# Performance work log

Measured on AMD Instinct MI355X. Metric: run time of the kernel, lower is better.

## Reference

```python
import jax, jax.numpy as jnp
import numpy as np

N_NODES = 100000
N_EDGES = 1200000
D = 64
N_REL = 50


def setup_inputs() -> dict:
    key = jax.random.key(0)
    ks = jax.random.split(key, 7)
    x = jax.random.normal(ks[0], (N_NODES, D), dtype=jnp.float32)
    rel_weight = jax.random.normal(ks[1], (N_REL, D), dtype=jnp.float32)
    loop_w1 = jax.random.normal(ks[2], (D, D), dtype=jnp.float32) * (1.0 / np.sqrt(D))
    loop_w2 = jax.random.normal(ks[3], (D, D), dtype=jnp.float32) * (1.0 / np.sqrt(D))
    src = jax.random.randint(ks[4], (N_EDGES,), 0, N_NODES, dtype=jnp.int32)
    dst = jax.random.randint(ks[5], (N_EDGES,), 0, N_NODES, dtype=jnp.int32)
    etype = jax.random.randint(ks[6], (N_EDGES,), 0, N_REL, dtype=jnp.int32)
    return {"x": x, "rel_weight": rel_weight, "loop_w1": loop_w1,
            "loop_w2": loop_w2, "src": src, "dst": dst, "etype": etype}


def _rgcn_layer(x, loop_w, rel_weight, src, dst, etype, n_nodes):
    # norm='both': pre-scale source feats by out_degree^-0.5
    ones_e = jnp.ones(src.shape[0], dtype=x.dtype)
    out_deg = jax.ops.segment_sum(ones_e, src, num_segments=n_nodes)
    in_deg = jax.ops.segment_sum(ones_e, dst, num_segments=n_nodes)
    norm_out = jnp.maximum(out_deg, 1.0) ** -0.5          # [N]
    h_src = x * norm_out[:, None]                          # [N, D]
    # per-edge: gather src feats + relation weights, elementwise multiply
    m = h_src[src] * rel_weight[etype]                     # [E, D]
    # scatter-mean over destination nodes
    msum = jax.ops.segment_sum(m, dst, num_segments=n_nodes)  # [N, D]
    mix = msum / jnp.maximum(in_deg, 1.0)[:, None]
    # self-loop dense matmul on dst feats (= original x)
    rst = x @ loop_w + mix
    # post-scale by in_degree^-0.5
    rst = rst * (jnp.maximum(in_deg, 1.0) ** -0.5)[:, None]
    return jax.nn.relu(rst)


def reference(x, rel_weight, loop_w1, loop_w2, src, dst, etype):
    n = x.shape[0]
    h = _rgcn_layer(x, loop_w1, rel_weight, src, dst, etype, n)
    h = _rgcn_layer(h, loop_w2, rel_weight, src, dst, etype, n)
    return h
```

## Files before the change

### kernel.cpp

```cpp
#include <hip/hip_runtime.h>


#define SCAN_BLK 1024

__global__ void deg_kernel(const int* __restrict__ src, const int* __restrict__ dst,
                           int* __restrict__ out_cnt, int* __restrict__ in_cnt, int E) {
  int i = blockIdx.x * blockDim.x + threadIdx.x;
  int stride = gridDim.x * blockDim.x;
  for (int e = i; e < E; e += stride) {
    atomicAdd(&out_cnt[src[e]], 1);
    atomicAdd(&in_cnt[dst[e]], 1);
  }
}

__global__ void scan_a(const int* __restrict__ in, int* __restrict__ out1,
                       int* __restrict__ bsums, int n) {
  __shared__ int tmp[SCAN_BLK];
  int i = blockIdx.x * SCAN_BLK + threadIdx.x;
  tmp[threadIdx.x] = (i < n) ? in[i] : 0;
  __syncthreads();
  for (int off = 1; off < SCAN_BLK; off <<= 1) {
    int t = (threadIdx.x >= off) ? tmp[threadIdx.x - off] : 0;
    __syncthreads();
    tmp[threadIdx.x] += t;
    __syncthreads();
  }
  if (i < n) out1[i] = tmp[threadIdx.x];
  if (threadIdx.x == SCAN_BLK - 1) bsums[blockIdx.x] = tmp[SCAN_BLK - 1];
}

__global__ void scan_b(const int* __restrict__ bsums, int* __restrict__ boff, int nb) {
  __shared__ int t[256];
  int v = (threadIdx.x < nb) ? bsums[threadIdx.x] : 0;
  t[threadIdx.x] = v;
  __syncthreads();
  for (int off = 1; off < 256; off <<= 1) {
    int u = (threadIdx.x >= off) ? t[threadIdx.x - off] : 0;
    __syncthreads();
    t[threadIdx.x] += u;
    __syncthreads();
  }
  if (threadIdx.x < nb) boff[threadIdx.x] = t[threadIdx.x] - v;
}

__global__ void scan_c(int* __restrict__ rowptr, const int* __restrict__ boff, int n) {
  int i = blockIdx.x * blockDim.x + threadIdx.x;
  if (i < n) rowptr[i + 1] += boff[i >> 10];
  if (i == 0) rowptr[0] = 0;
}

__global__ void norms_kernel(const int* __restrict__ out_cnt, const int* __restrict__ in_cnt,
                             const int* __restrict__ rowptr,
                             float4* __restrict__ nrm4, int* __restrict__ cursor, int n) {
  int i = blockIdx.x * blockDim.x + threadIdx.x;
  if (i < n) {
    float od = (float)max(out_cnt[i], 1);
    float id = (float)max(in_cnt[i], 1);
    float4 v;
    v.x = 1.0f / id;
    v.y = sqrtf(od);
    v.z = rsqrtf(id);
    v.w = rsqrtf(od);
    nrm4[i] = v;
    cursor[i] = rowptr[i];
  }
}

__global__ void prescale_kernel(const float4* __restrict__ x4, const float4* __restrict__ nrm4,
                                float4* __restrict__ xs4, int n16) {
  int i = blockIdx.x * blockDim.x + threadIdx.x;
  if (i < n16) {
    float no = nrm4[i >> 4].w;
    float4 v = x4[i];
    v.x *= no; v.y *= no; v.z *= no; v.w *= no;
    xs4[i] = v;
  }
}

__global__ void fill_csr(const int* __restrict__ src, const int* __restrict__ dst,
                         const int* __restrict__ et, int* __restrict__ cursor,
                         int* __restrict__ ce, int E) {
  int i = blockIdx.x * blockDim.x + threadIdx.x;
  int stride = gridDim.x * blockDim.x;
  for (int e = i; e < E; e += stride) {
    int d = dst[e];
    int pos = atomicAdd(&cursor[d], 1);
    ce[pos] = src[e] | (et[e] << 20);
  }
}

template <bool FINAL>
__launch_bounds__(256, 8)
__global__ void layer_kernel(const float* __restrict__ xs, const float* __restrict__ W,
                             const float* __restrict__ relw,
                             const int* __restrict__ rowptr, const int* __restrict__ ce,
                             const float4* __restrict__ nrm4,
                             float* __restrict__ xout, int n) {
  __shared__ float Wl[4096];
  {
    const float4* __restrict__ Wg = (const float4*)W;
    float4* Wl4 = (float4*)Wl;
    for (int i = threadIdx.x; i < 1024; i += 256) Wl4[i] = Wg[i];
  }
  __syncthreads();

  const int node = blockIdx.x * 4 + (threadIdx.x >> 6);
  if (node >= n) return;
  const int lane = threadIdx.x & 63;
  const int g = lane >> 4;
  const int l = lane & 15;

  const int rb = rowptr[node];
  const int re = rowptr[node + 1];
  const float4 nr = nrm4[node];

  const float4* __restrict__ xs4 = (const float4*)xs;
  const float4* __restrict__ rw4 = (const float4*)relw;

  float4 acc0 = {0.f, 0.f, 0.f, 0.f};
  float4 acc1 = {0.f, 0.f, 0.f, 0.f};
  int e = rb + g;
  for (; e + 4 < re; e += 8) {
    const int p0 = ce[e];
    const int p1 = ce[e + 4];
    const int s0 = p0 & 0xFFFFF, t0 = p0 >> 20;
    const int s1 = p1 & 0xFFFFF, t1 = p1 >> 20;
    const float4 xv0 = xs4[(size_t)s0 * 16 + l];
    const float4 xv1 = xs4[(size_t)s1 * 16 + l];
    const float4 rv0 = rw4[t0 * 16 + l];
    const float4 rv1 = rw4[t1 * 16 + l];
    acc0.x = fmaf(xv0.x, rv0.x, acc0.x);
    acc0.y = fmaf(xv0.y, rv0.y, acc0.y);
    acc0.z = fmaf(xv0.z, rv0.z, acc0.z);
    acc0.w = fmaf(xv0.w, rv0.w, acc0.w);
    acc1.x = fmaf(xv1.x, rv1.x, acc1.x);
    acc1.y = fmaf(xv1.y, rv1.y, acc1.y);
    acc1.z = fmaf(xv1.z, rv1.z, acc1.z);
    acc1.w = fmaf(xv1.w, rv1.w, acc1.w);
  }
  if (e < re) {
    const int p = ce[e];
    const int s = p & 0xFFFFF, t = p >> 20;
    const float4 xv = xs4[(size_t)s * 16 + l];
    const float4 rv = rw4[t * 16 + l];
    acc0.x = fmaf(xv.x, rv.x, acc0.x);
    acc0.y = fmaf(xv.y, rv.y, acc0.y);
    acc0.z = fmaf(xv.z, rv.z, acc0.z);
    acc0.w = fmaf(xv.w, rv.w, acc0.w);
  }
  float4 pre;
  pre.x = acc0.x + acc1.x;
  pre.y = acc0.y + acc1.y;
  pre.z = acc0.z + acc1.z;
  pre.w = acc0.w + acc1.w;

  pre.x += __shfl_xor(pre.x, 16); pre.x += __shfl_xor(pre.x, 32);
  pre.y += __shfl_xor(pre.y, 16); pre.y += __shfl_xor(pre.y, 32);
  pre.z += __shfl_xor(pre.z, 16); pre.z += __shfl_xor(pre.z, 32);
  pre.w += __shfl_xor(pre.w, 16); pre.w += __shfl_xor(pre.w, 32);

  const int srcl = lane >> 2;
  const float t0 = __shfl(pre.x, srcl);
  const float t1 = __shfl(pre.y, srcl);
  const float t2 = __shfl(pre.z, srcl);
  const float t3 = __shfl(pre.w, srcl);
  const float ea = (lane & 2) ? ((lane & 1) ? t3 : t2)
                              : ((lane & 1) ? t1 : t0);

  float d0 = 0.f, d1 = 0.f, d2 = 0.f, d3 = 0.f;
  const float* __restrict__ xrow = xs + (size_t)node * 64;
#pragma unroll
  for (int k = 0; k < 64; k += 4) {
    d0 = fmaf(xrow[k],     Wl[(k)     * 64 + lane], d0);
    d1 = fmaf(xrow[k + 1], Wl[(k + 1) * 64 + lane], d1);
    d2 = fmaf(xrow[k + 2], Wl[(k + 2) * 64 + lane], d2);
    d3 = fmaf(xrow[k + 3], Wl[(k + 3) * 64 + lane], d3);
  }
  const float dense = (d0 + d1) + (d2 + d3);

  const float scale = FINAL ? nr.z : nr.z * nr.w;
  const float r = fmaf(ea, nr.x, dense * nr.y) * scale;
  xout[(size_t)node * 64 + lane] = fmaxf(r, 0.f);
}

extern "C" void kernel_launch(void* const* d_in, const int* in_sizes, int n_in,
                              void* d_out, int out_size, void* d_ws, size_t ws_size,
                              hipStream_t stream) {
  const float* x     = (const float*)d_in[0];
  const float* relw  = (const float*)d_in[1];
  const float* w1    = (const float*)d_in[2];
  const float* w2    = (const float*)d_in[3];
  const int*   src   = (const int*)d_in[4];
  const int*   dst   = (const int*)d_in[5];
  const int*   etype = (const int*)d_in[6];

  const int N = in_sizes[0] / 64;
  const int E = in_sizes[4];

  char* w = (char*)d_ws;
  size_t off = 0;
  auto alloc = [&](size_t bytes) -> void* {
    void* p = w + off;
    off = (off + bytes + 255) & ~(size_t)255;
    return p;
  };
  int*    out_cnt = (int*)alloc((size_t)N * 4);
  int*    in_cnt  = (int*)alloc((size_t)N * 4);
  int*    rowptr  = (int*)alloc((size_t)(N + 1) * 4);
  int*    cursor  = (int*)alloc((size_t)N * 4);
  float4* nrm4    = (float4*)alloc((size_t)N * 16);
  int*    bsums   = (int*)alloc(256 * 4);
  int*    boff    = (int*)alloc(256 * 4);
  int*    ce      = (int*)alloc((size_t)E * 4);
  float*  xs      = (float*)alloc((size_t)N * 64 * 4);
  float*  h1s     = (float*)alloc((size_t)N * 64 * 4);

  hipMemsetAsync(out_cnt, 0, ((char*)rowptr - (char*)out_cnt), stream);

  const int nb = (N + SCAN_BLK - 1) / SCAN_BLK;

  deg_kernel<<<4096, 256, 0, stream>>>(src, dst, out_cnt, in_cnt, E);
  scan_a<<<nb, SCAN_BLK, 0, stream>>>(in_cnt, rowptr + 1, bsums, N);
  scan_b<<<1, 256, 0, stream>>>(bsums, boff, nb);
  scan_c<<<(N + 255) / 256, 256, 0, stream>>>(rowptr, boff, N);
  norms_kernel<<<(N + 255) / 256, 256, 0, stream>>>(out_cnt, in_cnt, rowptr, nrm4, cursor, N);
  prescale_kernel<<<(N * 16 + 255) / 256, 256, 0, stream>>>((const float4*)x, nrm4,
                                                            (float4*)xs, N * 16);
  fill_csr<<<4096, 256, 0, stream>>>(src, dst, etype, cursor, ce, E);

  const int lblocks = (N + 3) / 4;
  layer_kernel<false><<<lblocks, 256, 0, stream>>>(xs, w1, relw, rowptr, ce, nrm4, h1s, N);
  layer_kernel<true><<<lblocks, 256, 0, stream>>>(h1s, w2, relw, rowptr, ce, nrm4,
                                                  (float*)d_out, N);
}
```

Before: 465.4 us.

## Split self-loop matmul into separate register-resident kernel; merge scan fixup with norms

Moves the dense self-loop x@W product out of the gather layer kernel into a persistent kernel that holds one column of W in registers per lane and writes a pre-scaled intermediate y. The layer kernel then reads y instead of loading W into 16KB of shared memory per block, which removes the shared-memory staging and barrier and should allow higher occupancy for the latency-bound gather. It also fuses the scan fixup with the norms/cursor kernel by writing a separate rowfin array. The cost is two extra kernel launches and an extra N×64 float write and read per layer.

```diff
diff --git a/kernel.cpp b/kernel.cpp
--- a/kernel.cpp
+++ b/kernel.cpp
@@ -43,17 +43,16 @@
   if (threadIdx.x < nb) boff[threadIdx.x] = t[threadIdx.x] - v;
 }
 
-__global__ void scan_c(int* __restrict__ rowptr, const int* __restrict__ boff, int n) {
-  int i = blockIdx.x * blockDim.x + threadIdx.x;
-  if (i < n) rowptr[i + 1] += boff[i >> 10];
-  if (i == 0) rowptr[0] = 0;
-}
-
-__global__ void norms_kernel(const int* __restrict__ out_cnt, const int* __restrict__ in_cnt,
-                             const int* __restrict__ rowptr,
-                             float4* __restrict__ nrm4, int* __restrict__ cursor, int n) {
+__global__ void scan_c2(const int* __restrict__ rowptr, const int* __restrict__ boff,
+                        const int* __restrict__ out_cnt, const int* __restrict__ in_cnt,
+                        int* __restrict__ rowfin, int* __restrict__ cursor,
+                        float4* __restrict__ nrm4, int n) {
   int i = blockIdx.x * blockDim.x + threadIdx.x;
   if (i < n) {
+    rowfin[i + 1] = rowptr[i + 1] + boff[i >> 10];
+    int rp0 = (i == 0) ? 0 : rowptr[i] + boff[(i - 1) >> 10];
+    if (i == 0) rowfin[0] = 0;
+    cursor[i] = rp0;
     float od = (float)max(out_cnt[i], 1);
     float id = (float)max(in_cnt[i], 1);
     float4 v;
@@ -62,7 +61,6 @@
     v.z = rsqrtf(id);
     v.w = rsqrtf(od);
     nrm4[i] = v;
-    cursor[i] = rowptr[i];
   }
 }
 
@@ -89,21 +87,38 @@
   }
 }
 
+__launch_bounds__(256, 4)
+__global__ void selfloop_kernel(const float* __restrict__ xs, const float* __restrict__ W,
+                                const float4* __restrict__ nrm4,
+                                float* __restrict__ y, int n) {
+  const int lane = threadIdx.x & 63;
+  float wc[64];
+#pragma unroll
+  for (int k = 0; k < 64; ++k) wc[k] = W[k * 64 + lane];
+  const int wid = (blockIdx.x * blockDim.x + threadIdx.x) >> 6;
+  const int nw = (gridDim.x * blockDim.x) >> 6;
+  for (int node0 = wid; node0 < n; node0 += nw) {
+    const int node = __builtin_amdgcn_readfirstlane(node0);
+    const float* __restrict__ xrow = xs + (size_t)node * 64;
+    float d0 = 0.f, d1 = 0.f, d2 = 0.f, d3 = 0.f;
+#pragma unroll
+    for (int k = 0; k < 64; k += 4) {
+      d0 = fmaf(xrow[k],     wc[k],     d0);
+      d1 = fmaf(xrow[k + 1], wc[k + 1], d1);
+      d2 = fmaf(xrow[k + 2], wc[k + 2], d2);
+      d3 = fmaf(xrow[k + 3], wc[k + 3], d3);
+    }
+    y[(size_t)node * 64 + lane] = ((d0 + d1) + (d2 + d3)) * nrm4[node].y;
+  }
+}
+
 template <bool FINAL>
 __launch_bounds__(256, 8)
-__global__ void layer_kernel(const float* __restrict__ xs, const float* __restrict__ W,
+__global__ void layer_kernel(const float* __restrict__ xs, const float* __restrict__ y,
                              const float* __restrict__ relw,
                              const int* __restrict__ rowptr, const int* __restrict__ ce,
                              const float4* __restrict__ nrm4,
                              float* __restrict__ xout, int n) {
-  __shared__ float Wl[4096];
-  {
-    const float4* __restrict__ Wg = (const float4*)W;
-    float4* Wl4 = (float4*)Wl;
-    for (int i = threadIdx.x; i < 1024; i += 256) Wl4[i] = Wg[i];
-  }
-  __syncthreads();
-
   const int node = blockIdx.x * 4 + (threadIdx.x >> 6);
   if (node >= n) return;
   const int lane = threadIdx.x & 63;
@@ -167,19 +182,10 @@
   const float ea = (lane & 2) ? ((lane & 1) ? t3 : t2)
                               : ((lane & 1) ? t1 : t0);
 
-  float d0 = 0.f, d1 = 0.f, d2 = 0.f, d3 = 0.f;
-  const float* __restrict__ xrow = xs + (size_t)node * 64;
-#pragma unroll
-  for (int k = 0; k < 64; k += 4) {
-    d0 = fmaf(xrow[k],     Wl[(k)     * 64 + lane], d0);
-    d1 = fmaf(xrow[k + 1], Wl[(k + 1) * 64 + lane], d1);
-    d2 = fmaf(xrow[k + 2], Wl[(k + 2) * 64 + lane], d2);
-    d3 = fmaf(xrow[k + 3], Wl[(k + 3) * 64 + lane], d3);
-  }
-  const float dense = (d0 + d1) + (d2 + d3);
+  const float yv = y[(size_t)node * 64 + lane];
 
   const float scale = FINAL ? nr.z : nr.z * nr.w;
-  const float r = fmaf(ea, nr.x, dense * nr.y) * scale;
+  const float r = fmaf(ea, nr.x, yv) * scale;
   xout[(size_t)node * 64 + lane] = fmaxf(r, 0.f);
 }
 
@@ -207,6 +213,7 @@
   int*    out_cnt = (int*)alloc((size_t)N * 4);
   int*    in_cnt  = (int*)alloc((size_t)N * 4);
   int*    rowptr  = (int*)alloc((size_t)(N + 1) * 4);
+  int*    rowfin  = (int*)alloc((size_t)(N + 1) * 4);
   int*    cursor  = (int*)alloc((size_t)N * 4);
   float4* nrm4    = (float4*)alloc((size_t)N * 16);
   int*    bsums   = (int*)alloc(256 * 4);
@@ -214,6 +221,7 @@
   int*    ce      = (int*)alloc((size_t)E * 4);
   float*  xs      = (float*)alloc((size_t)N * 64 * 4);
   float*  h1s     = (float*)alloc((size_t)N * 64 * 4);
+  float*  y       = (float*)alloc((size_t)N * 64 * 4);
 
   hipMemsetAsync(out_cnt, 0, ((char*)rowptr - (char*)out_cnt), stream);
 
@@ -222,14 +230,16 @@
   deg_kernel<<<4096, 256, 0, stream>>>(src, dst, out_cnt, in_cnt, E);
   scan_a<<<nb, SCAN_BLK, 0, stream>>>(in_cnt, rowptr + 1, bsums, N);
   scan_b<<<1, 256, 0, stream>>>(bsums, boff, nb);
-  scan_c<<<(N + 255) / 256, 256, 0, stream>>>(rowptr, boff, N);
-  norms_kernel<<<(N + 255) / 256, 256, 0, stream>>>(out_cnt, in_cnt, rowptr, nrm4, cursor, N);
+  scan_c2<<<(N + 255) / 256, 256, 0, stream>>>(rowptr, boff, out_cnt, in_cnt,
+                                               rowfin, cursor, nrm4, N);
   prescale_kernel<<<(N * 16 + 255) / 256, 256, 0, stream>>>((const float4*)x, nrm4,
                                                             (float4*)xs, N * 16);
   fill_csr<<<4096, 256, 0, stream>>>(src, dst, etype, cursor, ce, E);
 
   const int lblocks = (N + 3) / 4;
-  layer_kernel<false><<<lblocks, 256, 0, stream>>>(xs, w1, relw, rowptr, ce, nrm4, h1s, N);
-  layer_kernel<true><<<lblocks, 256, 0, stream>>>(h1s, w2, relw, rowptr, ce, nrm4,
+  selfloop_kernel<<<4096, 256, 0, stream>>>(xs, w1, nrm4, y, N);
+  layer_kernel<false><<<lblocks, 256, 0, stream>>>(xs, y, relw, rowfin, ce, nrm4, h1s, N);
+  selfloop_kernel<<<4096, 256, 0, stream>>>(h1s, w2, nrm4, y, N);
+  layer_kernel<true><<<lblocks, 256, 0, stream>>>(h1s, y, relw, rowfin, ce, nrm4,
                                                   (float*)d_out, N);
 }
```

Result: faster. 439.7 us (-5.5%).
